# Kernel tuning notes

Measured on AMD Instinct MI355X. Metric: run time of the kernel, lower is better.

Reference implementation:

```python
import jax, jax.numpy as jnp
import numpy as np

NEG_SLOPE = 0.2  # PyG GATConv default leaky_relu slope
EPS = 1e-16


def gat_conv(x, src, dst, W, att_src, att_dst, bias, heads, concat):
    """PyG-style GATConv. x: [N, Fin]; W: [Fin, heads*C]; att_*: [heads, C].
    Edge (src j -> dst i): alpha_ij = softmax_i(leaky_relu(a_src.h_j + a_dst.h_i)).
    """
    N = x.shape[0]
    h = (x @ W).reshape(N, heads, -1)                       # [N, H, C]
    a_s = jnp.einsum('nhc,hc->nh', h, att_src)              # [N, H]
    a_d = jnp.einsum('nhc,hc->nh', h, att_dst)              # [N, H]
    e = jax.nn.leaky_relu(a_s[src] + a_d[dst], NEG_SLOPE)   # [E, H]
    # numerically stable segment softmax over incoming edges of each dst node
    e_max = jax.ops.segment_max(e, dst, num_segments=N)     # [N, H]
    e_max = jnp.where(jnp.isfinite(e_max), e_max, 0.0)      # isolated nodes
    ex = jnp.exp(e - e_max[dst])                            # [E, H]
    denom = jax.ops.segment_sum(ex, dst, num_segments=N)    # [N, H]
    alpha = ex / (denom[dst] + EPS)                         # [E, H]
    msg = alpha[:, :, None] * h[src]                        # [E, H, C]
    out = jax.ops.segment_sum(msg, dst, num_segments=N)     # [N, H, C]
    out = out.reshape(N, -1) if concat else out.mean(axis=1)
    return out + bias


def setup_inputs() -> dict:
    key = jax.random.key(0)
    ks = jax.random.split(key, 12)
    N, E = 100000, 1600000
    Fin, hidden, heads, Fout = 128, 128, 8, 64
    C1 = hidden // heads  # 16
    s = lambda f: 1.0 / np.sqrt(f)
    x = jax.random.normal(ks[0], (N, Fin), dtype=jnp.float32)
    edge_index = jax.random.randint(ks[1], (2, E), 0, N, dtype=jnp.int64)
    W1 = jax.random.normal(ks[2], (Fin, heads * C1), dtype=jnp.float32) * s(Fin)
    att_src1 = jax.random.normal(ks[3], (heads, C1), dtype=jnp.float32) * s(C1)
    att_dst1 = jax.random.normal(ks[4], (heads, C1), dtype=jnp.float32) * s(C1)
    b1 = jnp.zeros((hidden,), dtype=jnp.float32)
    W2 = jax.random.normal(ks[5], (hidden, Fout), dtype=jnp.float32) * s(hidden)
    att_src2 = jax.random.normal(ks[6], (1, Fout), dtype=jnp.float32) * s(Fout)
    att_dst2 = jax.random.normal(ks[7], (1, Fout), dtype=jnp.float32) * s(Fout)
    b2 = jnp.zeros((Fout,), dtype=jnp.float32)
    return {"x": x, "edge_index": edge_index,
            "W1": W1, "att_src1": att_src1, "att_dst1": att_dst1, "b1": b1,
            "W2": W2, "att_src2": att_src2, "att_dst2": att_dst2, "b2": b2}


def reference(x, edge_index, W1, att_src1, att_dst1, b1, W2, att_src2, att_dst2, b2):
    # eval mode: dropouts are identity
    src, dst = edge_index[0], edge_index[1]
    h = gat_conv(x, src, dst, W1, att_src1, att_dst1, b1, heads=8, concat=True)
    h = jax.nn.elu(h)
    out = gat_conv(h, src, dst, W2, att_src2, att_dst2, b2, heads=1, concat=False)
    return out
```

## Files before the change

### kernel.cpp

```cpp
#include <hip/hip_runtime.h>
#include <hip/hip_bf16.h>
#include <hip/hip_fp16.h>
#include <stdint.h>

#define SLOPE 0.2f
#define EPSV 1e-16f
#define LOG2E 1.44269504f
#define H1W 72
#define H2W 36

#define NPB2  256
#define NBLK  512

typedef __attribute__((ext_vector_type(8))) short bf16x8;
typedef __attribute__((ext_vector_type(4))) float f32x4;

static __device__ __forceinline__ uint32_t cvtpk(float a, float b) {
    uint32_t r;
    asm("v_cvt_pk_bf16_f32 %0, %1, %2" : "=v"(r) : "v"(a), "v"(b));
    return r;
}
static __device__ __forceinline__ float lof(uint32_t u) { return __uint_as_float(u << 16); }
static __device__ __forceinline__ float hif(uint32_t u) { return __uint_as_float(u & 0xffff0000u); }

static __device__ __forceinline__ uint32_t pkf16(float a, float b) {
    auto r = __builtin_amdgcn_cvt_pkrtz(a, b);
    return __builtin_bit_cast(uint32_t, r);
}

static __device__ __forceinline__ void fmix_lo(float& acc, uint32_t h2, float w) {
    asm("v_fma_mix_f32 %0, %1, %2, %0 op_sel_hi:[1,0,0]" : "+v"(acc) : "v"(h2), "v"(w));
}
static __device__ __forceinline__ void fmix_hi(float& acc, uint32_t h2, float w) {
    asm("v_fma_mix_f32 %0, %1, %2, %0 op_sel:[1,0,0] op_sel_hi:[1,0,0]" : "+v"(acc) : "v"(h2), "v"(w));
}

union FragCvt { uint4 u; bf16x8 f; };

__global__ __launch_bounds__(256) void gemm1_mfma(
    const float* __restrict__ x,
    const uint32_t* __restrict__ wthi, const uint32_t* __restrict__ wtlo,
    const float* __restrict__ att_src, const float* __restrict__ att_dst,
    uint32_t* __restrict__ h1p, float* __restrict__ ad1, int N)
{
    __shared__ uint32_t lds[2][128 * 36];
    const int t = threadIdx.x;
    const int w = t >> 6, l = t & 63;
    const int cl = l & 15, rg = l >> 4;
    const int rowbase = blockIdx.x * 128 + w * 32;

    f32x4 zero = {0.f, 0.f, 0.f, 0.f};
    f32x4 acc[2][8];
    #pragma unroll
    for (int rt = 0; rt < 2; ++rt)
        #pragma unroll
        for (int tl = 0; tl < 8; ++tl) acc[rt][tl] = zero;

    for (int kh = 0; kh < 2; ++kh) {
        if (kh) __syncthreads();
        for (int i = t; i < 1024; i += 256) {
            int col = i >> 3, q = i & 7;
            *(uint4*)&lds[0][col * 36 + q * 4] = *(const uint4*)&wthi[col * 64 + kh * 32 + q * 4];
            *(uint4*)&lds[1][col * 36 + q * 4] = *(const uint4*)&wtlo[col * 64 + kh * 32 + q * 4];
        }
        __syncthreads();
        #pragma unroll
        for (int ks = 0; ks < 2; ++ks) {
            const int kg = kh * 64 + ks * 32 + rg * 8;
            bf16x8 ahi[2], alo[2];
            #pragma unroll
            for (int rt = 0; rt < 2; ++rt) {
                int row = rowbase + rt * 16 + cl;
                row = min(row, N - 1);
                const float* xr = x + (size_t)row * 128 + kg;
                float4 v0 = *(const float4*)xr;
                float4 v1 = *(const float4*)(xr + 4);
                uint32_t h0 = cvtpk(v0.x, v0.y), h1 = cvtpk(v0.z, v0.w);
                uint32_t h2 = cvtpk(v1.x, v1.y), h3 = cvtpk(v1.z, v1.w);
                uint32_t l0 = cvtpk(v0.x - lof(h0), v0.y - hif(h0));
                uint32_t l1 = cvtpk(v0.z - lof(h1), v0.w - hif(h1));
                uint32_t l2 = cvtpk(v1.x - lof(h2), v1.y - hif(h2));
                uint32_t l3 = cvtpk(v1.z - lof(h3), v1.w - hif(h3));
                FragCvt ch, clo;
                ch.u  = make_uint4(h0, h1, h2, h3);
                clo.u = make_uint4(l0, l1, l2, l3);
                ahi[rt] = ch.f; alo[rt] = clo.f;
            }
            #pragma unroll
            for (int tl = 0; tl < 8; ++tl) {
                const int off = (tl * 16 + cl) * 36 + ks * 16 + rg * 4;
                bf16x8 bhi = *(const bf16x8*)&lds[0][off];
                bf16x8 blo = *(const bf16x8*)&lds[1][off];
                #pragma unroll
                for (int rt = 0; rt < 2; ++rt) {
                    acc[rt][tl] = __builtin_amdgcn_mfma_f32_16x16x32_bf16(alo[rt], bhi, acc[rt][tl], 0, 0, 0);
                    acc[rt][tl] = __builtin_amdgcn_mfma_f32_16x16x32_bf16(ahi[rt], blo, acc[rt][tl], 0, 0, 0);
                    acc[rt][tl] = __builtin_amdgcn_mfma_f32_16x16x32_bf16(ahi[rt], bhi, acc[rt][tl], 0, 0, 0);
                }
            }
        }
    }

    #pragma unroll
    for (int rt = 0; rt < 2; ++rt) {
        const int rowb = rowbase + rt * 16 + rg * 4;
        #pragma unroll
        for (int tl = 0; tl < 8; ++tl) {
            f32x4 a = acc[rt][tl];
            float as_ = att_src[tl * 16 + cl] * LOG2E, ad_ = att_dst[tl * 16 + cl] * LOG2E;
            float s0 = a.x * as_, s1 = a.y * as_, s2 = a.z * as_, s3 = a.w * as_;
            float d0 = a.x * ad_, d1 = a.y * ad_, d2 = a.z * ad_, d3 = a.w * ad_;
            #pragma unroll
            for (int off = 1; off < 16; off <<= 1) {
                s0 += __shfl_xor(s0, off); s1 += __shfl_xor(s1, off);
                s2 += __shfl_xor(s2, off); s3 += __shfl_xor(s3, off);
                d0 += __shfl_xor(d0, off); d1 += __shfl_xor(d1, off);
                d2 += __shfl_xor(d2, off); d3 += __shfl_xor(d3, off);
            }
            float av[4] = {a.x, a.y, a.z, a.w};
            #pragma unroll
            for (int r = 0; r < 4; ++r) {
                float partner = __shfl_xor(av[r], 1);
                if (!(cl & 1)) {
                    int row = rowb + r;
                    if (row < N)
                        h1p[(size_t)row * H1W + tl * 8 + (cl >> 1)] = pkf16(av[r], partner);
                }
            }
            if (cl == 0) {
                float sv[4] = {s0, s1, s2, s3}, dv[4] = {d0, d1, d2, d3};
                #pragma unroll
                for (int r = 0; r < 4; ++r) {
                    int row = rowb + r;
                    if (row < N) {
                        h1p[(size_t)row * H1W + 64 + tl] = __float_as_uint(sv[r]);
                        ad1[row * 8 + tl] = dv[r];
                    }
                }
            }
        }
    }
}

__global__ __launch_bounds__(256) void gemm2_mfma(
    const float* __restrict__ h,
    const uint32_t* __restrict__ wthi, const uint32_t* __restrict__ wtlo,
    const float* __restrict__ att_src, const float* __restrict__ att_dst,
    uint32_t* __restrict__ h2p, float* __restrict__ ad2, int N)
{
    __shared__ uint32_t lds[2][64 * 36];
    const int t = threadIdx.x;
    const int w = t >> 6, l = t & 63;
    const int cl = l & 15, rg = l >> 4;
    const int rowbase = blockIdx.x * 128 + w * 32;

    f32x4 zero = {0.f, 0.f, 0.f, 0.f};
    f32x4 acc[2][4];
    #pragma unroll
    for (int rt = 0; rt < 2; ++rt)
        #pragma unroll
        for (int tl = 0; tl < 4; ++tl) acc[rt][tl] = zero;

    for (int kh = 0; kh < 2; ++kh) {
        if (kh) __syncthreads();
        for (int i = t; i < 512; i += 256) {
            int col = i >> 3, q = i & 7;
            *(uint4*)&lds[0][col * 36 + q * 4] = *(const uint4*)&wthi[col * 64 + kh * 32 + q * 4];
            *(uint4*)&lds[1][col * 36 + q * 4] = *(const uint4*)&wtlo[col * 64 + kh * 32 + q * 4];
        }
        __syncthreads();
        #pragma unroll
        for (int ks = 0; ks < 2; ++ks) {
            const int kg = kh * 64 + ks * 32 + rg * 8;
            bf16x8 ahi[2], alo[2];
            #pragma unroll
            for (int rt = 0; rt < 2; ++rt) {
                int row = rowbase + rt * 16 + cl;
                row = min(row, N - 1);
                const float* xr = h + (size_t)row * 128 + kg;
                float4 v0 = *(const float4*)xr;
                float4 v1 = *(const float4*)(xr + 4);
                uint32_t h0 = cvtpk(v0.x, v0.y), h1 = cvtpk(v0.z, v0.w);
                uint32_t h2 = cvtpk(v1.x, v1.y), h3 = cvtpk(v1.z, v1.w);
                uint32_t l0 = cvtpk(v0.x - lof(h0), v0.y - hif(h0));
                uint32_t l1 = cvtpk(v0.z - lof(h1), v0.w - hif(h1));
                uint32_t l2 = cvtpk(v1.x - lof(h2), v1.y - hif(h2));
                uint32_t l3 = cvtpk(v1.z - lof(h3), v1.w - hif(h3));
                FragCvt ch, clo;
                ch.u  = make_uint4(h0, h1, h2, h3);
                clo.u = make_uint4(l0, l1, l2, l3);
                ahi[rt] = ch.f; alo[rt] = clo.f;
            }
            #pragma unroll
            for (int tl = 0; tl < 4; ++tl) {
                const int off = (tl * 16 + cl) * 36 + ks * 16 + rg * 4;
                bf16x8 bhi = *(const bf16x8*)&lds[0][off];
                bf16x8 blo = *(const bf16x8*)&lds[1][off];
                #pragma unroll
                for (int rt = 0; rt < 2; ++rt) {
                    acc[rt][tl] = __builtin_amdgcn_mfma_f32_16x16x32_bf16(alo[rt], bhi, acc[rt][tl], 0, 0, 0);
                    acc[rt][tl] = __builtin_amdgcn_mfma_f32_16x16x32_bf16(ahi[rt], blo, acc[rt][tl], 0, 0, 0);
                    acc[rt][tl] = __builtin_amdgcn_mfma_f32_16x16x32_bf16(ahi[rt], bhi, acc[rt][tl], 0, 0, 0);
                }
            }
        }
    }

    #pragma unroll
    for (int rt = 0; rt < 2; ++rt) {
        const int rowb = rowbase + rt * 16 + rg * 4;
        float s0 = 0.f, s1 = 0.f, s2 = 0.f, s3 = 0.f;
        float d0 = 0.f, d1 = 0.f, d2 = 0.f, d3 = 0.f;
        #pragma unroll
        for (int tl = 0; tl < 4; ++tl) {
            f32x4 a = acc[rt][tl];
            float as_ = att_src[tl * 16 + cl] * LOG2E, ad_ = att_dst[tl * 16 + cl] * LOG2E;
            s0 += a.x * as_; s1 += a.y * as_; s2 += a.z * as_; s3 += a.w * as_;
            d0 += a.x * ad_; d1 += a.y * ad_; d2 += a.z * ad_; d3 += a.w * ad_;
            float av[4] = {a.x, a.y, a.z, a.w};
            #pragma unroll
            for (int r = 0; r < 4; ++r) {
                float partner = __shfl_xor(av[r], 1);
                if (!(cl & 1)) {
                    int row = rowb + r;
                    if (row < N)
                        h2p[(size_t)row * H2W + tl * 8 + (cl >> 1)] = pkf16(av[r], partner);
                }
            }
        }
        #pragma unroll
        for (int off = 1; off < 16; off <<= 1) {
            s0 += __shfl_xor(s0, off); s1 += __shfl_xor(s1, off);
            s2 += __shfl_xor(s2, off); s3 += __shfl_xor(s3, off);
            d0 += __shfl_xor(d0, off); d1 += __shfl_xor(d1, off);
            d2 += __shfl_xor(d2, off); d3 += __shfl_xor(d3, off);
        }
        if (cl == 0) {
            float sv[4] = {s0, s1, s2, s3}, dv[4] = {d0, d1, d2, d3};
            #pragma unroll
            for (int r = 0; r < 4; ++r) {
                int row = rowb + r;
                if (row < N) {
                    h2p[(size_t)row * H2W + 32] = __float_as_uint(sv[r]);
                    ad2[row] = dv[r];
                }
            }
        }
    }
}

__global__ __launch_bounds__(256) void s_count(
    const int* __restrict__ ei, int* __restrict__ pbh, int E, int NB, int chunk,
    const float* __restrict__ W1, const float* __restrict__ W2,
    uint32_t* __restrict__ wt1hi, uint32_t* __restrict__ wt1lo,
    uint32_t* __restrict__ wt2hi, uint32_t* __restrict__ wt2lo)
{
    int t = threadIdx.x;
    if (blockIdx.x >= NBLK) {
        if (blockIdx.x == NBLK) {
            for (int i = t; i < 128 * 64; i += 256) {
                int n = i >> 6, kp = i & 63;
                float w0 = W1[(2 * kp) * 128 + n], w1 = W1[(2 * kp + 1) * 128 + n];
                uint32_t h = cvtpk(w0, w1);
                wt1hi[n * 64 + kp] = h;
                wt1lo[n * 64 + kp] = cvtpk(w0 - lof(h), w1 - hif(h));
            }
        } else {
            for (int i = t; i < 64 * 64; i += 256) {
                int n = i >> 6, kp = i & 63;
                float w0 = W2[(2 * kp) * 64 + n], w1 = W2[(2 * kp + 1) * 64 + n];
                uint32_t h = cvtpk(w0, w1);
                wt2hi[n * 64 + kp] = h;
                wt2lo[n * 64 + kp] = cvtpk(w0 - lof(h), w1 - hif(h));
            }
        }
        return;
    }
    __shared__ int hist[512];
    hist[t] = 0; hist[t + 256] = 0;
    __syncthreads();
    int e0 = blockIdx.x * chunk, e1 = min(E, e0 + chunk);
    for (int e = e0 + t; e < e1; e += 256)
        atomicAdd(&hist[ei[E + e] >> 8], 1);
    __syncthreads();
    for (int b = t; b < NB; b += 256)
        pbh[(size_t)b * NBLK + blockIdx.x] = hist[b];
}

__global__ __launch_bounds__(256) void s_scanA(
    const int* __restrict__ pbh, int* __restrict__ btot, int NB)
{
    __shared__ int red[256];
    int b = blockIdx.x, t = threadIdx.x;
    int s = pbh[(size_t)b * NBLK + t] + pbh[(size_t)b * NBLK + 256 + t];
    red[t] = s; __syncthreads();
    for (int off = 128; off; off >>= 1) {
        if (t < off) red[t] += red[t + off];
        __syncthreads();
    }
    if (t == 0) btot[b] = red[0];
}

__global__ __launch_bounds__(256) void s_scanC(
    int* __restrict__ pbh, const int* __restrict__ btot,
    int* __restrict__ bucket_base, int NB, int E)
{
    __shared__ int ps[256];
    __shared__ int exv[512];
    int b = blockIdx.x, t = threadIdx.x;
    int v0 = (2 * t     < NB) ? btot[2 * t]     : 0;
    int v1 = (2 * t + 1 < NB) ? btot[2 * t + 1] : 0;
    int p = v0 + v1;
    ps[t] = p; __syncthreads();
    for (int off = 1; off < 256; off <<= 1) {
        int add = (t >= off) ? ps[t - off] : 0;
        __syncthreads();
        ps[t] += add;
        __syncthreads();
    }
    int pex = ps[t] - p;
    exv[2 * t] = pex; exv[2 * t + 1] = pex + v0;
    __syncthreads();
    int base = exv[b];
    if (t == 0) {
        bucket_base[b] = base;
        if (b == NB - 1) bucket_base[NB] = E;
    }
    __syncthreads();
    int w0 = pbh[(size_t)b * NBLK + 2 * t], w1 = pbh[(size_t)b * NBLK + 2 * t + 1];
    int pp = w0 + w1;
    ps[t] = pp; __syncthreads();
    for (int off = 1; off < 256; off <<= 1) {
        int add = (t >= off) ? ps[t - off] : 0;
        __syncthreads();
        ps[t] += add;
        __syncthreads();
    }
    int ex = base + ps[t] - pp;
    pbh[(size_t)b * NBLK + 2 * t]     = ex;
    pbh[(size_t)b * NBLK + 2 * t + 1] = ex + w0;
}

__global__ __launch_bounds__(256) void s_place(
    const int* __restrict__ ei, const int* __restrict__ pbh,
    uint32_t* __restrict__ staging, int E, int NB, int chunk)
{
    __shared__ int lcur[512];
    int t = threadIdx.x;
    if (t < NB)       lcur[t]       = pbh[(size_t)t * NBLK + blockIdx.x];
    if (t + 256 < NB) lcur[t + 256] = pbh[(size_t)(t + 256) * NBLK + blockIdx.x];
    __syncthreads();
    int e0 = blockIdx.x * chunk, e1 = min(E, e0 + chunk);
    for (int e = e0 + t; e < e1; e += 256) {
        int s = ei[e], d = ei[E + e];
        int p = atomicAdd(&lcur[d >> 8], 1);
        staging[p] = ((uint32_t)s << 8) | (uint32_t)(d & 255);
    }
}

__global__ __launch_bounds__(256) void s_build(
    const uint32_t* __restrict__ staging, const int* __restrict__ bucket_base,
    int* __restrict__ row_start, int* __restrict__ sorted_src, int N, int E, int NB)
{
    __shared__ int cnt[256];
    __shared__ int ofs[256];
    __shared__ int ps[256];
    int b = blockIdx.x, t = threadIdx.x;
    int base = bucket_base[b], end = bucket_base[b + 1];
    cnt[t] = 0;
    __syncthreads();
    for (int i = base + t; i < end; i += 256)
        atomicAdd(&cnt[staging[i] & 255], 1);
    __syncthreads();
    int c = cnt[t];
    ps[t] = c; __syncthreads();
    for (int off = 1; off < 256; off <<= 1) {
        int add = (t >= off) ? ps[t - off] : 0;
        __syncthreads();
        ps[t] += add;
        __syncthreads();
    }
    int ex = ps[t] - c;
    ofs[t] = ex;
    int node = b * NPB2 + t;
    if (node < N) row_start[node] = base + ex;
    if (b == NB - 1 && t == 0) row_start[N] = E;
    __syncthreads();
    for (int i = base + t; i < end; i += 256) {
        uint32_t v = staging[i];
        int pos = base + atomicAdd(&ofs[v & 255], 1);
        sorted_src[pos] = (int)(v >> 8);
    }
}

__global__ __launch_bounds__(256) void gather1_kernel(
    const int* __restrict__ row_start, const int* __restrict__ sorted_src,
    const float* __restrict__ ad1, const uint32_t* __restrict__ h1p,
    const float* __restrict__ b1, float* __restrict__ hbuf, int N)
{
    int node = blockIdx.x * 4 + (threadIdx.x >> 6);
    if (node >= N) return;
    const int l  = threadIdx.x & 63;
    const int wh = l & 7;
    const int eA = l >> 3;
    const int c8 = l & 15;
    const int q  = l >> 4;
    const int hB = c8 >> 1;

    int r0 = row_start[node], r1 = row_start[node + 1];

    if (r0 == r1) {
        if (l < 16) {
            #pragma unroll
            for (int g = 0; g < 2; ++g) {
                float4 bv = *(const float4*)&b1[c8 * 8 + g * 4];
                bv.x = bv.x > 0.f ? bv.x : expm1f(bv.x);
                bv.y = bv.y > 0.f ? bv.y : expm1f(bv.y);
                bv.z = bv.z > 0.f ? bv.z : expm1f(bv.z);
                bv.w = bv.w > 0.f ? bv.w : expm1f(bv.w);
                *(float4*)&hbuf[(size_t)node * 128 + c8 * 8 + g * 4] = bv;
            }
        }
        return;
    }

    float adw = ad1[node * 8 + wh];
    const uint32_t* rowp = h1p + 4 * c8;
    float acc[8] = {0.f, 0.f, 0.f, 0.f, 0.f, 0.f, 0.f, 0.f};
    float den = 0.f;

    int jw = r0 + eA;
    int sw0 = sorted_src[jw < r1 ? jw : r0] * H1W;
    int j1 = r0 + 8 + eA;
    int sw1 = sorted_src[j1 < r1 ? j1 : r0] * H1W;
    float av0 = __uint_as_float(h1p[sw0 + 64 + wh]);

    int of0A = __shfl(sw0,  q      * 8, 64);
    int of1A = __shfl(sw0, (q + 4) * 8, 64);
    uint4 hA0 = *(const uint4*)(rowp + of0A);
    uint4 hA1 = *(const uint4*)(rowp + of1A);

    for (int j = r0; j < r1; j += 8) {
        int jn = j + 16 + eA;
        int swn = sorted_src[jn < r1 ? jn : r0] * H1W;
        float avn = __uint_as_float(h1p[sw1 + 64 + wh]);

        int of0B = __shfl(sw1,  q      * 8, 64);
        int of1B = __shfl(sw1, (q + 4) * 8, 64);
        uint4 hB0 = *(const uint4*)(rowp + of0B);
        uint4 hB1 = *(const uint4*)(rowp + of1B);

        float ev = av0 + adw;
        ev = ev > 0.f ? ev : SLOPE * ev;
        float w = (j + eA) < r1 ? exp2f(ev) : 0.f;
        den += w;

        float wk0 = __shfl(w,  q      * 8 + hB, 64);
        float wk1 = __shfl(w, (q + 4) * 8 + hB, 64);
        fmix_lo(acc[0], hA0.x, wk0); fmix_hi(acc[1], hA0.x, wk0);
        fmix_lo(acc[2], hA0.y, wk0); fmix_hi(acc[3], hA0.y, wk0);
        fmix_lo(acc[4], hA0.z, wk0); fmix_hi(acc[5], hA0.z, wk0);
        fmix_lo(acc[6], hA0.w, wk0); fmix_hi(acc[7], hA0.w, wk0);
        fmix_lo(acc[0], hA1.x, wk1); fmix_hi(acc[1], hA1.x, wk1);
        fmix_lo(acc[2], hA1.y, wk1); fmix_hi(acc[3], hA1.y, wk1);
        fmix_lo(acc[4], hA1.z, wk1); fmix_hi(acc[5], hA1.z, wk1);
        fmix_lo(acc[6], hA1.w, wk1); fmix_hi(acc[7], hA1.w, wk1);

        hA0 = hB0; hA1 = hB1;
        sw0 = sw1; sw1 = swn; av0 = avn;
    }

    den += __shfl_xor(den, 8, 64);
    den += __shfl_xor(den, 16, 64);
    den += __shfl_xor(den, 32, 64);
    float dB = __shfl(den, hB, 64);

    #pragma unroll
    for (int i = 0; i < 8; ++i) {
        acc[i] += __shfl_xor(acc[i], 16, 64);
        acc[i] += __shfl_xor(acc[i], 32, 64);
    }

    if (l < 16) {
        float inv = 1.0f / (dB + EPSV);
        #pragma unroll
        for (int g = 0; g < 2; ++g) {
            float4 bv = *(const float4*)&b1[c8 * 8 + g * 4];
            float v0 = acc[g * 4 + 0] * inv + bv.x;
            float v1 = acc[g * 4 + 1] * inv + bv.y;
            float v2 = acc[g * 4 + 2] * inv + bv.z;
            float v3 = acc[g * 4 + 3] * inv + bv.w;
            v0 = v0 > 0.f ? v0 : expm1f(v0);
            v1 = v1 > 0.f ? v1 : expm1f(v1);
            v2 = v2 > 0.f ? v2 : expm1f(v2);
            v3 = v3 > 0.f ? v3 : expm1f(v3);
            *(float4*)&hbuf[(size_t)node * 128 + c8 * 8 + g * 4] = make_float4(v0, v1, v2, v3);
        }
    }
}

__global__ __launch_bounds__(256) void gather2_kernel(
    const int* __restrict__ row_start, const int* __restrict__ sorted_src,
    const float* __restrict__ ad2, const uint32_t* __restrict__ h2p,
    const float* __restrict__ b2, float* __restrict__ out, int N)
{
    int node = blockIdx.x * 8 + (threadIdx.x >> 5);
    if (node >= N) return;
    const int l  = threadIdx.x & 31;
    const int eA = l & 7;
    const int c8 = l & 7;
    const int q  = l >> 3;

    int r0 = row_start[node], r1 = row_start[node + 1];

    if (r0 == r1) {
        if (l < 8) {
            #pragma unroll
            for (int g = 0; g < 2; ++g) {
                float4 bv = *(const float4*)&b2[c8 * 8 + g * 4];
                *(float4*)&out[(size_t)node * 64 + c8 * 8 + g * 4] = bv;
            }
        }
        return;
    }

    float ad = ad2[node];
    const uint32_t* rowp = h2p + 4 * c8;
    float acc[8] = {0.f, 0.f, 0.f, 0.f, 0.f, 0.f, 0.f, 0.f};
    float den = 0.f;

    int jw = r0 + eA;
    int sw0 = sorted_src[jw < r1 ? jw : r0] * H2W;
    int j1 = r0 + 8 + eA;
    int sw1 = sorted_src[j1 < r1 ? j1 : r0] * H2W;
    float av0 = __uint_as_float(h2p[sw0 + 32]);

    int of0A = __shfl(sw0, q,     32);
    int of1A = __shfl(sw0, q + 4, 32);
    uint4 hA0 = *(const uint4*)(rowp + of0A);
    uint4 hA1 = *(const uint4*)(rowp + of1A);

    for (int j = r0; j < r1; j += 8) {
        int jn = j + 16 + eA;
        int swn = sorted_src[jn < r1 ? jn : r0] * H2W;
        float avn = __uint_as_float(h2p[sw1 + 32]);

        int of0B = __shfl(sw1, q,     32);
        int of1B = __shfl(sw1, q + 4, 32);
        uint4 hB0 = *(const uint4*)(rowp + of0B);
        uint4 hB1 = *(const uint4*)(rowp + of1B);

        float ev = av0 + ad;
        ev = ev > 0.f ? ev : SLOPE * ev;
        float w = (j + eA) < r1 ? exp2f(ev) : 0.f;
        den += w;

        float wk0 = __shfl(w, q,     32);
        float wk1 = __shfl(w, q + 4, 32);
        fmix_lo(acc[0], hA0.x, wk0); fmix_hi(acc[1], hA0.x, wk0);
        fmix_lo(acc[2], hA0.y, wk0); fmix_hi(acc[3], hA0.y, wk0);
        fmix_lo(acc[4], hA0.z, wk0); fmix_hi(acc[5], hA0.z, wk0);
        fmix_lo(acc[6], hA0.w, wk0); fmix_hi(acc[7], hA0.w, wk0);
        fmix_lo(acc[0], hA1.x, wk1); fmix_hi(acc[1], hA1.x, wk1);
        fmix_lo(acc[2], hA1.y, wk1); fmix_hi(acc[3], hA1.y, wk1);
        fmix_lo(acc[4], hA1.z, wk1); fmix_hi(acc[5], hA1.z, wk1);
        fmix_lo(acc[6], hA1.w, wk1); fmix_hi(acc[7], hA1.w, wk1);

        hA0 = hB0; hA1 = hB1;
        sw0 = sw1; sw1 = swn; av0 = avn;
    }

    den += __shfl_xor(den, 1, 32);
    den += __shfl_xor(den, 2, 32);
    den += __shfl_xor(den, 4, 32);
    #pragma unroll
    for (int i = 0; i < 8; ++i) {
        acc[i] += __shfl_xor(acc[i], 8, 32);
        acc[i] += __shfl_xor(acc[i], 16, 32);
    }

    if (l < 8) {
        float inv = 1.0f / (den + EPSV);
        #pragma unroll
        for (int g = 0; g < 2; ++g) {
            float4 bv = *(const float4*)&b2[c8 * 8 + g * 4];
            *(float4*)&out[(size_t)node * 64 + c8 * 8 + g * 4] =
                make_float4(acc[g * 4 + 0] * inv + bv.x, acc[g * 4 + 1] * inv + bv.y,
                            acc[g * 4 + 2] * inv + bv.z, acc[g * 4 + 3] * inv + bv.w);
        }
    }
}

extern "C" void kernel_launch(void* const* d_in, const int* in_sizes, int n_in,
                              void* d_out, int out_size, void* d_ws, size_t ws_size,
                              hipStream_t stream)
{
    const int N = in_sizes[0] / 128;
    const int E = in_sizes[1] / 2;
    const int NB = (N + NPB2 - 1) / NPB2;
    const int chunk = (E + NBLK - 1) / NBLK;

    const float* x        = (const float*)d_in[0];
    const int*   ei       = (const int*)  d_in[1];
    const float* W1       = (const float*)d_in[2];
    const float* att_src1 = (const float*)d_in[3];
    const float* att_dst1 = (const float*)d_in[4];
    const float* b1       = (const float*)d_in[5];
    const float* W2       = (const float*)d_in[6];
    const float* att_src2 = (const float*)d_in[7];
    const float* att_dst2 = (const float*)d_in[8];
    const float* b2       = (const float*)d_in[9];
    float* out = (float*)d_out;

    uint32_t* h1p  = (uint32_t*)d_ws;
    float* hbuf    = (float*)(h1p + (size_t)N * H1W);
    float* ad1     = hbuf + (size_t)N * 128;
    float* ad2     = ad1  + (size_t)N * 8;
    int* row_start   = (int*)(ad2 + N);
    int* bucket_base = row_start + (N + 1);
    int* btot        = bucket_base + (NB + 1);
    int* pbh         = btot + NB;
    int* sorted_src  = pbh + (size_t)NB * NBLK;
    uint32_t* staging = (uint32_t*)(sorted_src + E);
    uint32_t* wt1hi = staging + E;
    uint32_t* wt1lo = wt1hi + 128 * 64;
    uint32_t* wt2hi = wt1lo + 128 * 64;
    uint32_t* wt2lo = wt2hi + 64 * 64;
    uint32_t* h2p   = h1p;

    s_count<<<NBLK + 2, 256, 0, stream>>>(ei, pbh, E, NB, chunk,
                                          W1, W2, wt1hi, wt1lo, wt2hi, wt2lo);
    s_scanA<<<NB, 256, 0, stream>>>(pbh, btot, NB);
    s_scanC<<<NB, 256, 0, stream>>>(pbh, btot, bucket_base, NB, E);
    s_place<<<NBLK, 256, 0, stream>>>(ei, pbh, staging, E, NB, chunk);
    s_build<<<NB, 256, 0, stream>>>(staging, bucket_base, row_start, sorted_src, N, E, NB);

    gemm1_mfma<<<(N + 127) / 128, 256, 0, stream>>>(x, wt1hi, wt1lo, att_src1, att_dst1, h1p, ad1, N);
    gather1_kernel<<<(N + 3) / 4, 256, 0, stream>>>(row_start, sorted_src, ad1, h1p, b1, hbuf, N);

    gemm2_mfma<<<(N + 127) / 128, 256, 0, stream>>>(hbuf, wt2hi, wt2lo, att_src2, att_dst2, h2p, ad2, N);
    gather2_kernel<<<(N + 7) / 8, 256, 0, stream>>>(row_start, sorted_src, ad2, h2p, b2, out, N);
}
```

Measured before the change: 249.4 us.

## Fuse edge-count histogram with GEMM1 and convert weights per block in LDS

Merges the destination-bucket histogram kernel and the first MFMA GEMM into one launch, with the first NBLK blocks doing counting and the rest doing GEMM, which removes one kernel launch and lets the two independent jobs overlap. The separate weight pre-transposition into bf16 hi/lo buffers is dropped. Each GEMM block now reads fp32 W directly and splits it into hi/lo while filling LDS. This adds redundant per-block weight conversion and strided global reads of W in exchange for fewer launches and less workspace traffic.

```diff
diff --git a/kernel.cpp b/kernel.cpp
--- a/kernel.cpp
+++ b/kernel.cpp
@@ -37,17 +37,32 @@
 
 union FragCvt { uint4 u; bf16x8 f; };
 
-__global__ __launch_bounds__(256) void gemm1_mfma(
-    const float* __restrict__ x,
-    const uint32_t* __restrict__ wthi, const uint32_t* __restrict__ wtlo,
+__global__ __launch_bounds__(256) void fused_count_gemm1(
+    const int* __restrict__ ei, int* __restrict__ pbh, int E, int NB, int chunk,
+    const float* __restrict__ x, const float* __restrict__ W1,
     const float* __restrict__ att_src, const float* __restrict__ att_dst,
-    uint32_t* __restrict__ h1p, float* __restrict__ ad1, int N)
+    uint32_t* __restrict__ h1p, float* __restrict__ ad1, int N, int nCnt)
 {
     __shared__ uint32_t lds[2][128 * 36];
     const int t = threadIdx.x;
+
+    if (blockIdx.x < nCnt) {
+        int* hist = (int*)&lds[0][0];
+        hist[t] = 0; hist[t + 256] = 0;
+        __syncthreads();
+        int e0 = blockIdx.x * chunk, e1 = min(E, e0 + chunk);
+        for (int e = e0 + t; e < e1; e += 256)
+            atomicAdd(&hist[ei[E + e] >> 8], 1);
+        __syncthreads();
+        for (int b = t; b < NB; b += 256)
+            pbh[(size_t)b * NBLK + blockIdx.x] = hist[b];
+        return;
+    }
+
+    const int bx = blockIdx.x - nCnt;
     const int w = t >> 6, l = t & 63;
     const int cl = l & 15, rg = l >> 4;
-    const int rowbase = blockIdx.x * 128 + w * 32;
+    const int rowbase = bx * 128 + w * 32;
 
     f32x4 zero = {0.f, 0.f, 0.f, 0.f};
     f32x4 acc[2][8];
@@ -58,10 +73,14 @@
 
     for (int kh = 0; kh < 2; ++kh) {
         if (kh) __syncthreads();
-        for (int i = t; i < 1024; i += 256) {
-            int col = i >> 3, q = i & 7;
-            *(uint4*)&lds[0][col * 36 + q * 4] = *(const uint4*)&wthi[col * 64 + kh * 32 + q * 4];
-            *(uint4*)&lds[1][col * 36 + q * 4] = *(const uint4*)&wtlo[col * 64 + kh * 32 + q * 4];
+        for (int i = t; i < 4096; i += 256) {
+            int col = i & 127, kp = i >> 7;
+            int k0 = 2 * (kh * 32 + kp);
+            float w0 = W1[(size_t)k0 * 128 + col];
+            float w1 = W1[(size_t)(k0 + 1) * 128 + col];
+            uint32_t h = cvtpk(w0, w1);
+            lds[0][col * 36 + kp] = h;
+            lds[1][col * 36 + kp] = cvtpk(w0 - lof(h), w1 - hif(h));
         }
         __syncthreads();
         #pragma unroll
@@ -143,8 +162,7 @@
 }
 
 __global__ __launch_bounds__(256) void gemm2_mfma(
-    const float* __restrict__ h,
-    const uint32_t* __restrict__ wthi, const uint32_t* __restrict__ wtlo,
+    const float* __restrict__ h, const float* __restrict__ W2,
     const float* __restrict__ att_src, const float* __restrict__ att_dst,
     uint32_t* __restrict__ h2p, float* __restrict__ ad2, int N)
 {
@@ -163,10 +181,14 @@
 
     for (int kh = 0; kh < 2; ++kh) {
         if (kh) __syncthreads();
-        for (int i = t; i < 512; i += 256) {
-            int col = i >> 3, q = i & 7;
-            *(uint4*)&lds[0][col * 36 + q * 4] = *(const uint4*)&wthi[col * 64 + kh * 32 + q * 4];
-            *(uint4*)&lds[1][col * 36 + q * 4] = *(const uint4*)&wtlo[col * 64 + kh * 32 + q * 4];
+        for (int i = t; i < 2048; i += 256) {
+            int col = i & 63, kp = i >> 6;
+            int k0 = 2 * (kh * 32 + kp);
+            float w0 = W2[(size_t)k0 * 64 + col];
+            float w1 = W2[(size_t)(k0 + 1) * 64 + col];
+            uint32_t hh = cvtpk(w0, w1);
+            lds[0][col * 36 + kp] = hh;
+            lds[1][col * 36 + kp] = cvtpk(w0 - lof(hh), w1 - hif(hh));
         }
         __syncthreads();
         #pragma unroll
@@ -249,44 +271,6 @@
     }
 }
 
-__global__ __launch_bounds__(256) void s_count(
-    const int* __restrict__ ei, int* __restrict__ pbh, int E, int NB, int chunk,
-    const float* __restrict__ W1, const float* __restrict__ W2,
-    uint32_t* __restrict__ wt1hi, uint32_t* __restrict__ wt1lo,
-    uint32_t* __restrict__ wt2hi, uint32_t* __restrict__ wt2lo)
-{
-    int t = threadIdx.x;
-    if (blockIdx.x >= NBLK) {
-        if (blockIdx.x == NBLK) {
-            for (int i = t; i < 128 * 64; i += 256) {
-                int n = i >> 6, kp = i & 63;
-                float w0 = W1[(2 * kp) * 128 + n], w1 = W1[(2 * kp + 1) * 128 + n];
-                uint32_t h = cvtpk(w0, w1);
-                wt1hi[n * 64 + kp] = h;
-                wt1lo[n * 64 + kp] = cvtpk(w0 - lof(h), w1 - hif(h));
-            }
-        } else {
-            for (int i = t; i < 64 * 64; i += 256) {
-                int n = i >> 6, kp = i & 63;
-                float w0 = W2[(2 * kp) * 64 + n], w1 = W2[(2 * kp + 1) * 64 + n];
-                uint32_t h = cvtpk(w0, w1);
-                wt2hi[n * 64 + kp] = h;
-                wt2lo[n * 64 + kp] = cvtpk(w0 - lof(h), w1 - hif(h));
-            }
-        }
-        return;
-    }
-    __shared__ int hist[512];
-    hist[t] = 0; hist[t + 256] = 0;
-    __syncthreads();
-    int e0 = blockIdx.x * chunk, e1 = min(E, e0 + chunk);
-    for (int e = e0 + t; e < e1; e += 256)
-        atomicAdd(&hist[ei[E + e] >> 8], 1);
-    __syncthreads();
-    for (int b = t; b < NB; b += 256)
-        pbh[(size_t)b * NBLK + blockIdx.x] = hist[b];
-}
-
 __global__ __launch_bounds__(256) void s_scanA(
     const int* __restrict__ pbh, int* __restrict__ btot, int NB)
 {
@@ -599,6 +583,7 @@
     const int E = in_sizes[1] / 2;
     const int NB = (N + NPB2 - 1) / NPB2;
     const int chunk = (E + NBLK - 1) / NBLK;
+    const int gBlocks = (N + 127) / 128;
 
     const float* x        = (const float*)d_in[0];
     const int*   ei       = (const int*)  d_in[1];
@@ -622,22 +607,18 @@
     int* pbh         = btot + NB;
     int* sorted_src  = pbh + (size_t)NB * NBLK;
     uint32_t* staging = (uint32_t*)(sorted_src + E);
-    uint32_t* wt1hi = staging + E;
-    uint32_t* wt1lo = wt1hi + 128 * 64;
-    uint32_t* wt2hi = wt1lo + 128 * 64;
-    uint32_t* wt2lo = wt2hi + 64 * 64;
     uint32_t* h2p   = h1p;
 
-    s_count<<<NBLK + 2, 256, 0, stream>>>(ei, pbh, E, NB, chunk,
-                                          W1, W2, wt1hi, wt1lo, wt2hi, wt2lo);
+    fused_count_gemm1<<<NBLK + gBlocks, 256, 0, stream>>>(
+        ei, pbh, E, NB, chunk, x, W1, att_src1, att_dst1, h1p, ad1, N, NBLK);
+
     s_scanA<<<NB, 256, 0, stream>>>(pbh, btot, NB);
     s_scanC<<<NB, 256, 0, stream>>>(pbh, btot, bucket_base, NB, E);
     s_place<<<NBLK, 256, 0, stream>>>(ei, pbh, staging, E, NB, chunk);
     s_build<<<NB, 256, 0, stream>>>(staging, bucket_base, row_start, sorted_src, N, E, NB);
 
-    gemm1_mfma<<<(N + 127) / 128, 256, 0, stream>>>(x, wt1hi, wt1lo, att_src1, att_dst1, h1p, ad1, N);
     gather1_kernel<<<(N + 3) / 4, 256, 0, stream>>>(row_start, sorted_src, ad1, h1p, b1, hbuf, N);
 
-    gemm2_mfma<<<(N + 127) / 128, 256, 0, stream>>>(hbuf, wt2hi, wt2lo, att_src2, att_dst2, h2p, ad2, N);
+    gemm2_mfma<<<(N + 127) / 128, 256, 0, stream>>>(hbuf, W2, att_src2, att_dst2, h2p, ad2, N);
     gather2_kernel<<<(N + 7) / 8, 256, 0, stream>>>(row_start, sorted_src, ad2, h2p, b2, out, N);
 }
```

Measured after the change: 256.0 us. 2.7% more time.
